# Kernel optimization log

Hardware: AMD Instinct MI355X
Metric: run time of the kernel (lower is better)

Reference implementation:

```python
import jax, jax.numpy as jnp
import numpy as np

EPS = 1e-5

def conv2d(x, w, b=None, pad=1):
    # x: [B,C,H,W], w: [O,I,kh,kw]
    y = jax.lax.conv_general_dilated(x, w, (1, 1), [(pad, pad), (pad, pad)],
                                     dimension_numbers=('NCHW', 'OIHW', 'NCHW'))
    if b is not None:
        y = y + b[None, :, None, None]
    return y

def bn(x, g, b, m, v):
    # inference-mode batchnorm
    inv = g / jnp.sqrt(v + EPS)
    return x * inv[None, :, None, None] + (b - m * inv)[None, :, None, None]

def coord_conv(x, w, b):
    B, C, H, W = x.shape
    yy = jnp.broadcast_to(jnp.linspace(-1.0, 1.0, H)[:, None], (H, W))
    xx = jnp.broadcast_to(jnp.linspace(-1.0, 1.0, W)[None, :], (H, W))
    coords = jnp.broadcast_to(jnp.stack([xx, yy])[None], (B, 2, H, W)).astype(x.dtype)
    return conv2d(jnp.concatenate([x, coords], axis=1), w, b, pad=1)

def deform_conv(x, offset, w):
    # deformable conv v1, 3x3, pad=1, stride=1, no bias
    B, C, H, W = x.shape
    K = 9
    # offset channels interleaved (y, x) per kernel tap
    off = offset.reshape(B, K, 2, H, W)
    off_y, off_x = off[:, :, 0], off[:, :, 1]          # [B,9,H,W]
    k = jnp.arange(K)
    ko_y = (k // 3 - 1).astype(x.dtype)[None, :, None, None]
    ko_x = (k % 3 - 1).astype(x.dtype)[None, :, None, None]
    base_y = jnp.arange(H, dtype=x.dtype)[None, None, :, None]
    base_x = jnp.arange(W, dtype=x.dtype)[None, None, None, :]
    py = base_y + ko_y + off_y                          # [B,9,H,W]
    px = base_x + ko_x + off_x
    xf = x.reshape(B, C, H * W)
    y0 = jnp.floor(py)
    x0 = jnp.floor(px)
    acc = jnp.zeros((B, C, K, H, W), x.dtype)
    for dy in (0.0, 1.0):
        for dx in (0.0, 1.0):
            yy = y0 + dy
            xx = x0 + dx
            wgt = (1.0 - jnp.abs(py - yy)) * (1.0 - jnp.abs(px - xx))
            valid = (yy >= 0) & (yy < H) & (xx >= 0) & (xx < W)
            wgt = jnp.where(valid, wgt, 0.0)            # zero padding OOB
            yi = jnp.clip(yy, 0, H - 1).astype(jnp.int32)
            xi = jnp.clip(xx, 0, W - 1).astype(jnp.int32)
            idx = (yi * W + xi).reshape(B, K * H * W)
            v = jnp.take_along_axis(xf, idx[:, None, :], axis=2).reshape(B, C, K, H, W)
            acc = acc + v * wgt[:, None]
    wk = w.reshape(w.shape[0], w.shape[1], K)           # [O,I,9]
    return jnp.einsum('bckhw,ock->bohw', acc, wk)

def setup_inputs() -> dict:
    key = jax.random.key(0)
    ks = jax.random.split(key, 16)
    d_model, hd = 256, 64
    B, H, W = 8, 96, 96
    f32 = jnp.float32
    def bn_params(k):
        k1, k2, k3 = jax.random.split(k, 3)
        return (1.0 + 0.1 * jax.random.normal(k1, (hd,), f32),
                0.1 * jax.random.normal(k2, (hd,), f32),
                0.1 * jax.random.normal(k3, (hd,), f32),
                0.5 + jax.random.uniform(jax.random.fold_in(k, 7), (hd,), f32))
    bn1 = bn_params(ks[1]); bn2 = bn_params(ks[2]); bn3 = bn_params(ks[3]); bn4 = bn_params(ks[4])
    inp = {
        'features': jax.random.normal(ks[0], (B, H, W, d_model), f32),
        'coord_w': 0.05 * jax.random.normal(ks[5], (hd, d_model + 2, 3, 3), f32),
        'coord_b': jnp.zeros((hd,), f32),
        'bn1_g': bn1[0], 'bn1_b': bn1[1], 'bn1_m': bn1[2], 'bn1_v': bn1[3],
        'off_w': 0.01 * jax.random.normal(ks[6], (18, hd, 3, 3), f32),
        'off_b': 0.01 * jax.random.normal(ks[7], (18,), f32),
        'dc_w': 0.05 * jax.random.normal(ks[8], (hd, hd, 3, 3), f32),
        'bn2_g': bn2[0], 'bn2_b': bn2[1], 'bn2_m': bn2[2], 'bn2_v': bn2[3],
        'r1_w': 0.05 * jax.random.normal(ks[9], (hd, hd, 3, 3), f32),
        'bn3_g': bn3[0], 'bn3_b': bn3[1], 'bn3_m': bn3[2], 'bn3_v': bn3[3],
        'r2_w': 0.05 * jax.random.normal(ks[10], (hd, hd, 3, 3), f32),
        'bn4_g': bn4[0], 'bn4_b': bn4[1], 'bn4_m': bn4[2], 'bn4_v': bn4[3],
        'out_w': 0.1 * jax.random.normal(ks[11], (1, hd, 1, 1), f32),
        'out_b': jnp.zeros((1,), f32),
    }
    return inp

def reference(features, coord_w, coord_b, bn1_g, bn1_b, bn1_m, bn1_v,
              off_w, off_b, dc_w, bn2_g, bn2_b, bn2_m, bn2_v,
              r1_w, bn3_g, bn3_b, bn3_m, bn3_v,
              r2_w, bn4_g, bn4_b, bn4_m, bn4_v, out_w, out_b):
    x = jnp.transpose(features, (0, 3, 1, 2))           # NHWC -> NCHW
    x = jax.nn.relu(bn(coord_conv(x, coord_w, coord_b), bn1_g, bn1_b, bn1_m, bn1_v))
    offset = conv2d(x, off_w, off_b, pad=1)
    x = deform_conv(x, offset, dc_w)
    x = jax.nn.relu(bn(x, bn2_g, bn2_b, bn2_m, bn2_v))
    x = jax.nn.relu(bn(conv2d(x, r1_w, None, pad=1), bn3_g, bn3_b, bn3_m, bn3_v))
    x = jax.nn.relu(bn(conv2d(x, r2_w, None, pad=1), bn4_g, bn4_b, bn4_m, bn4_v))
    return jax.nn.sigmoid(conv2d(x, out_w, out_b, pad=0))
```

## Files before the change

kernel.cpp:

```cpp
#include <hip/hip_runtime.h>


typedef unsigned short u16;
typedef unsigned int u32;
typedef __attribute__((ext_vector_type(8)))  short bf16x8;
typedef __attribute__((ext_vector_type(16))) float f32x16;

#define EPSBN 1e-5f

__device__ __forceinline__ u16 f2bf(float f) {
  u32 u = __builtin_bit_cast(u32, f);
  u32 r = u + 0x7FFFu + ((u >> 16) & 1u);
  return (u16)(r >> 16);
}
__device__ __forceinline__ u32 pk2(float a, float b) {
  return (u32)f2bf(a) | ((u32)f2bf(b) << 16);
}
__device__ __forceinline__ float lo2f(u32 w) { return __builtin_bit_cast(float, w << 16); }
__device__ __forceinline__ float hi2f(u32 w) { return __builtin_bit_cast(float, w & 0xFFFF0000u); }

__device__ __forceinline__ void gload_lds16(const void* g, void* l) {
  __builtin_amdgcn_global_load_lds(
      (const __attribute__((address_space(1))) unsigned int*)g,
      (__attribute__((address_space(3))) unsigned int*)l, 16, 0, 0);
}

#define N_WCF 147456
#define N_WCC 9216
#define N_WOF 18432
#define N_W64 36864
#define N_ALLW (N_WCF + N_WCC + N_WOF + 3*N_W64)

#define FBK_BLOCKS 9216
#define WT_BLOCKS  1116

__global__ __launch_bounds__(256) void prep_kernel(
    const float* __restrict__ feat,
    const float* __restrict__ coord_w, const float* __restrict__ off_w,
    const float* __restrict__ dc_w, const float* __restrict__ r1_w,
    const float* __restrict__ r2_w,
    u16* __restrict__ fb,
    u16* __restrict__ wcf, u16* __restrict__ wcc, u16* __restrict__ wof,
    u16* __restrict__ wdf, u16* __restrict__ wr1, u16* __restrict__ wr2,
    u32* __restrict__ zb)
{
  const int t = threadIdx.x;
  if (blockIdx.x < FBK_BLOCKS) {
    const int e = (blockIdx.x * 256 + t) * 8;
    const float4 f0 = *(const float4*)(feat + e);
    const float4 f1 = *(const float4*)(feat + e + 4);
    uint4 o;
    o.x = pk2(f0.x, f0.y); o.y = pk2(f0.z, f0.w);
    o.z = pk2(f1.x, f1.y); o.w = pk2(f1.z, f1.w);
    *(uint4*)(fb + e) = o;
    return;
  }
  int i = (blockIdx.x - FBK_BLOCKS) * 256 + t;
  if (i < 64) zb[i] = 0u;
  if (i >= N_ALLW) return;
  int d = i;
  if (d < N_WCF) {
    int j = d & 7, lane = (d >> 3) & 63, frag = d >> 9;
    int nt = frag & 1, h = (frag >> 1) & 3, tap = (frag >> 3) % 9, cc = (frag >> 3) / 9;
    int ic = cc * 64 + h * 16 + ((lane >> 5) << 3) + j;
    int oc = nt * 32 + (lane & 31);
    wcf[d] = f2bf(coord_w[((size_t)oc * 258 + ic) * 9 + tap]);
    return;
  }
  d -= N_WCF;
  if (d < N_WCC) {
    int j = d & 7, lane = (d >> 3) & 63, frag = d >> 9;
    int nt = frag & 1, tap = frag >> 1;
    int ic = 256 + ((lane >> 5) << 3) + j;
    int oc = nt * 32 + (lane & 31);
    wcc[d] = (ic < 258) ? f2bf(coord_w[((size_t)oc * 258 + ic) * 9 + tap]) : (u16)0;
    return;
  }
  d -= N_WCC;
  if (d < N_WOF) {
    int j = d & 7, lane = (d >> 3) & 63, frag = d >> 9;
    int h = frag & 3, tap = frag >> 2;
    int ic = h * 16 + ((lane >> 5) << 3) + j;
    int oc = lane & 31;
    wof[d] = (oc < 18) ? f2bf(off_w[((size_t)oc * 64 + ic) * 9 + tap]) : (u16)0;
    return;
  }
  d -= N_WOF;
  int seg = d / N_W64;
  int e = d - seg * N_W64;
  int j = e & 7, lane = (e >> 3) & 63, frag = e >> 9;
  int nt = frag & 1, h = (frag >> 1) & 3, tap = frag >> 3;
  int ic = h * 16 + ((lane >> 5) << 3) + j;
  int oc = nt * 32 + (lane & 31);
  const float* src = (seg == 0) ? dc_w : (seg == 1) ? r1_w : r2_w;
  u16* dst = (seg == 0) ? wdf : (seg == 1) ? wr1 : wr2;
  dst[e] = f2bf(src[((size_t)oc * 64 + ic) * 9 + tap]);
}

__device__ __forceinline__ u32 stage_desc(int slot, int x0, int y0, int b,
                                          int px_stride) {
  const int px = slot / 9, part = slot - px * 9;
  if (part >= 8 || px >= 204) return 0xFFFFFFFFu;
  const int ly = px / 34, lx = px - ly * 34;
  const int gy = y0 + ly - 1, gx = x0 + lx - 1;
  if ((unsigned)gy >= 96u || (unsigned)gx >= 96u) return 0xFFFFFFFFu;
  return (u32)(((b * 96 + gy) * 96 + gx) * px_stride + part * 16);
}

__global__ __launch_bounds__(256, 4) void coord_conv_kernel(
    const u16* __restrict__ fb, const u16* __restrict__ wcf,
    const u16* __restrict__ wcc, const float* __restrict__ cb,
    const float* __restrict__ g, const float* __restrict__ bb,
    const float* __restrict__ m, const float* __restrict__ v,
    u16* __restrict__ x1b, const u32* __restrict__ zb)
{
  __shared__ __align__(16) u16 tile[16384];
  __shared__ __align__(16) u16 ct[204 * 16];
  const int t = threadIdx.x;
  const int wv = t >> 6, lane = t & 63;
  const int l31 = lane & 31, l5 = lane >> 5;
  const int rp = wv & 1, kh = wv >> 1;
  const int x0 = blockIdx.x * 32, y0 = blockIdx.y * 4, b = blockIdx.z;

  u32 desc[8];
  #pragma unroll
  for (int k = 0; k < 8; ++k)
    desc[k] = stage_desc((wv + 4 * k) * 64 + lane, x0, y0, b, 512);

  if (t < 204) {
    const int ly = t / 34, lx = t - ly * 34;
    const int gy = y0 + ly - 1, gx = x0 + lx - 1;
    uint4 o0 = {0u, 0u, 0u, 0u}, o1 = {0u, 0u, 0u, 0u};
    if ((unsigned)gy < 96u && (unsigned)gx < 96u) {
      const float xx = -1.f + (2.f / 95.f) * (float)gx;
      const float yy = -1.f + (2.f / 95.f) * (float)gy;
      o0.x = pk2(xx, yy);
    }
    *(uint4*)(ct + t * 16) = o0;
    *(uint4*)(ct + t * 16 + 8) = o1;
  }

  f32x16 acc[2][2] = {};

  for (int cc = 0; cc < 4; ++cc) {
    #pragma unroll
    for (int k = 0; k < 8; ++k) {
      const char* src = (desc[k] == 0xFFFFFFFFu)
          ? (const char*)zb : (const char*)fb + desc[k] + cc * 128;
      gload_lds16(src, (char*)tile + (wv + 4 * k) * 1024);
    }
    __syncthreads();
    #pragma unroll
    for (int tap = 0; tap < 9; ++tap) {
      const int dy = tap / 3, dx = tap - dy * 3;
      #pragma unroll
      for (int hh = 0; hh < 2; ++hh) {
        const int h = kh * 2 + hh;
        const bf16x8 a0 = *(const bf16x8*)(tile +
            ((rp * 2 + 0 + dy) * 34 + l31 + dx) * 72 + h * 16 + l5 * 8);
        const bf16x8 a1 = *(const bf16x8*)(tile +
            ((rp * 2 + 1 + dy) * 34 + l31 + dx) * 72 + h * 16 + l5 * 8);
        #pragma unroll
        for (int nt = 0; nt < 2; ++nt) {
          const bf16x8 bfr = *(const bf16x8*)(wcf +
              ((size_t)((((cc * 9 + tap) * 4 + h) * 2) + nt)) * 512 + lane * 8);
          acc[0][nt] = __builtin_amdgcn_mfma_f32_32x32x16_bf16(a0, bfr,
                                                               acc[0][nt], 0, 0, 0);
          acc[1][nt] = __builtin_amdgcn_mfma_f32_32x32x16_bf16(a1, bfr,
                                                               acc[1][nt], 0, 0, 0);
        }
      }
    }
    __syncthreads();
  }

  if (kh == 0) {
    #pragma unroll
    for (int tap = 0; tap < 9; ++tap) {
      const int dy = tap / 3, dx = tap - dy * 3;
      const bf16x8 a0 = *(const bf16x8*)(ct +
          ((rp * 2 + 0 + dy) * 34 + l31 + dx) * 16 + l5 * 8);
      const bf16x8 a1 = *(const bf16x8*)(ct +
          ((rp * 2 + 1 + dy) * 34 + l31 + dx) * 16 + l5 * 8);
      #pragma unroll
      for (int nt = 0; nt < 2; ++nt) {
        const bf16x8 bfr = *(const bf16x8*)(wcc +
            ((size_t)(tap * 2 + nt)) * 512 + lane * 8);
        acc[0][nt] = __builtin_amdgcn_mfma_f32_32x32x16_bf16(a0, bfr,
                                                             acc[0][nt], 0, 0, 0);
        acc[1][nt] = __builtin_amdgcn_mfma_f32_32x32x16_bf16(a1, bfr,
                                                             acc[1][nt], 0, 0, 0);
      }
    }
  }

  float* redk = (float*)tile;
  __syncthreads();
  if (kh == 1) {
    #pragma unroll
    for (int ai = 0; ai < 2; ++ai)
      #pragma unroll
      for (int nt = 0; nt < 2; ++nt)
        #pragma unroll
        for (int r = 0; r < 16; ++r)
          redk[(((rp * 2 + ai) * 2 + nt) * 16 + r) * 64 + lane] = acc[ai][nt][r];
  }
  __syncthreads();
  if (kh == 0) {
    #pragma unroll
    for (int ai = 0; ai < 2; ++ai)
      #pragma unroll
      for (int nt = 0; nt < 2; ++nt) {
        #pragma unroll
        for (int r = 0; r < 16; ++r)
          acc[ai][nt][r] += redk[(((rp * 2 + ai) * 2 + nt) * 16 + r) * 64 + lane];
        const int oc = nt * 32 + l31;
        const float inv = g[oc] * rsqrtf(v[oc] + EPSBN);
        const float sh = bb[oc] - m[oc] * inv + cb[oc] * inv;
        const int y = y0 + rp * 2 + ai;
        #pragma unroll
        for (int r = 0; r < 16; ++r) {
          const int xr = (r & 3) + 8 * (r >> 2) + 4 * l5;
          const float val = fmaxf(fmaf(acc[ai][nt][r], inv, sh), 0.f);
          x1b[((size_t)((b * 96 + y) * 96 + x0 + xr)) * 64 + oc] = f2bf(val);
        }
      }
  }
}

template<int NN, int EPI>
__global__ __launch_bounds__(256, 4) void conv64_kernel(
    const u16* __restrict__ xin, const u16* __restrict__ wf,
    const float* __restrict__ bias,
    const float* __restrict__ g, const float* __restrict__ bb,
    const float* __restrict__ m, const float* __restrict__ v,
    const float* __restrict__ ow, const float* __restrict__ ob,
    void* __restrict__ outp, const u32* __restrict__ zb)
{
  __shared__ __align__(16) u16 tile[16384];
  __shared__ float red2[128];
  const int t = threadIdx.x;
  const int wv = t >> 6, lane = t & 63;
  const int l31 = lane & 31, l5 = lane >> 5;
  const int rp = wv & 1, kh = wv >> 1;
  const int x0 = blockIdx.x * 32, y0 = blockIdx.y * 4, b = blockIdx.z;

  #pragma unroll
  for (int k = 0; k < 8; ++k) {
    const u32 d = stage_desc((wv + 4 * k) * 64 + lane, x0, y0, b, 128);
    const char* src = (d == 0xFFFFFFFFu) ? (const char*)zb
                                         : (const char*)xin + d;
    gload_lds16(src, (char*)tile + (wv + 4 * k) * 1024);
  }
  __syncthreads();

  f32x16 acc[2][NN] = {};
  #pragma unroll
  for (int tap = 0; tap < 9; ++tap) {
    const int dy = tap / 3, dx = tap - dy * 3;
    #pragma unroll
    for (int hh = 0; hh < 2; ++hh) {
      const int h = kh * 2 + hh;
      const bf16x8 a0 = *(const bf16x8*)(tile +
          ((rp * 2 + 0 + dy) * 34 + l31 + dx) * 72 + h * 16 + l5 * 8);
      const bf16x8 a1 = *(const bf16x8*)(tile +
          ((rp * 2 + 1 + dy) * 34 + l31 + dx) * 72 + h * 16 + l5 * 8);
      #pragma unroll
      for (int nt = 0; nt < NN; ++nt) {
        const size_t f = (NN == 2) ? (size_t)((tap * 4 + h) * 2 + nt)
                                   : (size_t)(tap * 4 + h);
        const bf16x8 bfr = *(const bf16x8*)(wf + f * 512 + lane * 8);
        acc[0][nt] = __builtin_amdgcn_mfma_f32_32x32x16_bf16(a0, bfr,
                                                             acc[0][nt], 0, 0, 0);
        acc[1][nt] = __builtin_amdgcn_mfma_f32_32x32x16_bf16(a1, bfr,
                                                             acc[1][nt], 0, 0, 0);
      }
    }
  }

  float* redk = (float*)tile;
  __syncthreads();
  if (kh == 1) {
    #pragma unroll
    for (int ai = 0; ai < 2; ++ai)
      #pragma unroll
      for (int nt = 0; nt < NN; ++nt)
        #pragma unroll
        for (int r = 0; r < 16; ++r)
          redk[(((rp * 2 + ai) * NN + nt) * 16 + r) * 64 + lane] = acc[ai][nt][r];
  }
  __syncthreads();

  if constexpr (EPI == 0) {
    if (kh == 0) {
      u16* xo = (u16*)outp;
      #pragma unroll
      for (int ai = 0; ai < 2; ++ai)
        #pragma unroll
        for (int nt = 0; nt < NN; ++nt) {
          #pragma unroll
          for (int r = 0; r < 16; ++r)
            acc[ai][nt][r] += redk[(((rp * 2 + ai) * NN + nt) * 16 + r) * 64 + lane];
          const int oc = nt * 32 + l31;
          const float inv = g[oc] * rsqrtf(v[oc] + EPSBN);
          const float sh = bb[oc] - m[oc] * inv;
          const int y = y0 + rp * 2 + ai;
          #pragma unroll
          for (int r = 0; r < 16; ++r) {
            const int xr = (r & 3) + 8 * (r >> 2) + 4 * l5;
            const float val = fmaxf(fmaf(acc[ai][nt][r], inv, sh), 0.f);
            xo[((size_t)((b * 96 + y) * 96 + x0 + xr)) * 64 + oc] = f2bf(val);
          }
        }
    }
  } else if constexpr (EPI == 1) {
    if (kh == 0) {
      float* fo = (float*)outp;
      #pragma unroll
      for (int ai = 0; ai < 2; ++ai) {
        #pragma unroll
        for (int r = 0; r < 16; ++r)
          acc[ai][0][r] += redk[(((rp * 2 + ai) * NN + 0) * 16 + r) * 64 + lane];
        if (l31 < 18) {
          const float bs = bias[l31];
          const int y = y0 + rp * 2 + ai;
          #pragma unroll
          for (int r = 0; r < 16; ++r) {
            const int xr = (r & 3) + 8 * (r >> 2) + 4 * l5;
            fo[((size_t)((b * 96 + y) * 96 + x0 + xr)) * 18 + l31] =
                acc[ai][0][r] + bs;
          }
        }
      }
    }
  } else {
    if (kh == 0) {
      #pragma unroll
      for (int ai = 0; ai < 2; ++ai) {
        float pr[16];
        #pragma unroll
        for (int r = 0; r < 16; ++r) pr[r] = 0.f;
        #pragma unroll
        for (int nt = 0; nt < NN; ++nt) {
          const int oc = nt * 32 + l31;
          const float inv = g[oc] * rsqrtf(v[oc] + EPSBN);
          const float sh = bb[oc] - m[oc] * inv;
          const float wo = ow[oc];
          #pragma unroll
          for (int r = 0; r < 16; ++r) {
            const float a = acc[ai][nt][r] +
                redk[(((rp * 2 + ai) * NN + nt) * 16 + r) * 64 + lane];
            const float val = fmaxf(fmaf(a, inv, sh), 0.f);
            pr[r] = fmaf(val, wo, pr[r]);
          }
        }
        #pragma unroll
        for (int mask = 1; mask <= 16; mask <<= 1)
          #pragma unroll
          for (int r = 0; r < 16; ++r)
            pr[r] += __shfl_xor(pr[r], mask);
        if (l31 == 0) {
          #pragma unroll
          for (int r = 0; r < 16; ++r) {
            const int xr = (r & 3) + 8 * (r >> 2) + 4 * l5;
            red2[(rp * 2 + ai) * 32 + xr] = pr[r];
          }
        }
      }
    }
    __syncthreads();
    if (t < 128) {
      float* fo = (float*)outp;
      const int yy = y0 + (t >> 5), xx = x0 + (t & 31);
      const float val = red2[t] + ob[0];
      fo[(size_t)(b * 96 + yy) * 96 + xx] = 1.f / (1.f + expf(-val));
    }
  }
}

__global__ __launch_bounds__(512, 4) void deform_kernel(
    const u16* __restrict__ x1b, const float* __restrict__ off,
    const u16* __restrict__ wdf,
    const float* __restrict__ g, const float* __restrict__ bb,
    const float* __restrict__ m, const float* __restrict__ v,
    u16* __restrict__ x2b)
{
  __shared__ __align__(16) u16 s[2 * 128 * 72];
  __shared__ float offs[128 * 18];
  const int t = threadIdx.x;
  const int wv = t >> 6, lane = t & 63;
  const int l31 = lane & 31, l5 = lane >> 5;
  const int mt = wv & 3, ntw = wv >> 2;
  const int x0 = blockIdx.x * 16, y0 = blockIdx.y * 8, b = blockIdx.z;

  {
    float po[5];
    #pragma unroll
    for (int r = 0; r < 5; ++r) {
      const int i = t + r * 512;
      po[r] = 0.f;
      if (i < 2304) {
        const int p = i / 18, c = i - p * 18;
        const int gy = y0 + (p >> 4), gx = x0 + (p & 15);
        po[r] = off[((size_t)((b * 96 + gy) * 96 + gx)) * 18 + c];
      }
    }
    #pragma unroll
    for (int r = 0; r < 5; ++r) {
      const int i = t + r * 512;
      if (i < 2304) offs[i] = po[r];
    }
  }
  __syncthreads();

  const int sp = t >> 2, part = t & 3;
  const int sy = y0 + (sp >> 4), sx = x0 + (sp & 15);

  uint4 gbuf[8];
  float w4[4];

  auto prefetch = [&](int k) {
    const float oy = offs[sp * 18 + 2 * k];
    const float ox = offs[sp * 18 + 2 * k + 1];
    const float py = (float)(sy + k / 3 - 1) + oy;
    const float px = (float)(sx + k % 3 - 1) + ox;
    const float yf = floorf(py), xf = floorf(px);
    const float fy = py - yf, fx = px - xf;
    const int yi = (int)yf, xi = (int)xf;
    #pragma unroll
    for (int cor = 0; cor < 4; ++cor) {
      const int cy = yi + (cor >> 1), cx = xi + (cor & 1);
      const uint4 z = {0u, 0u, 0u, 0u};
      gbuf[2 * cor] = z; gbuf[2 * cor + 1] = z;
      const float wy = (cor & 2) ? fy : 1.f - fy;
      const float wx = (cor & 1) ? fx : 1.f - fx;
      w4[cor] = 0.f;
      if ((unsigned)cy < 96u && (unsigned)cx < 96u) {
        w4[cor] = wy * wx;
        const u16* p = x1b + ((size_t)((b * 96 + cy) * 96 + cx)) * 64
                       + part * 16;
        gbuf[2 * cor]     = *(const uint4*)p;
        gbuf[2 * cor + 1] = *(const uint4*)(p + 8);
      }
    }
  };
  auto combine = [&](u16* dst) {
    float val[16];
    #pragma unroll
    for (int j = 0; j < 16; ++j) val[j] = 0.f;
    #pragma unroll
    for (int cor = 0; cor < 4; ++cor) {
      const float wgt = w4[cor];
      const u32 uu[8] = {gbuf[2 * cor].x, gbuf[2 * cor].y,
                         gbuf[2 * cor].z, gbuf[2 * cor].w,
                         gbuf[2 * cor + 1].x, gbuf[2 * cor + 1].y,
                         gbuf[2 * cor + 1].z, gbuf[2 * cor + 1].w};
      #pragma unroll
      for (int u = 0; u < 8; ++u) {
        val[2 * u]     = fmaf(wgt, lo2f(uu[u]), val[2 * u]);
        val[2 * u + 1] = fmaf(wgt, hi2f(uu[u]), val[2 * u + 1]);
      }
    }
    u32 pk[8];
    #pragma unroll
    for (int u = 0; u < 8; ++u) pk[u] = pk2(val[2 * u], val[2 * u + 1]);
    uint4 w0 = {pk[0], pk[1], pk[2], pk[3]};
    uint4 w1 = {pk[4], pk[5], pk[6], pk[7]};
    *(uint4*)(dst + sp * 72 + part * 16) = w0;
    *(uint4*)(dst + sp * 72 + part * 16 + 8) = w1;
  };

  f32x16 acc = {};

  prefetch(0);
  combine(s);
  __syncthreads();

  for (int k = 0; k < 9; ++k) {
    u16* cur = s + (k & 1) * 9216;
    if (k < 8) prefetch(k + 1);
    #pragma unroll
    for (int h = 0; h < 4; ++h) {
      const bf16x8 afr = *(const bf16x8*)(cur + (mt * 32 + l31) * 72
                                          + h * 16 + l5 * 8);
      const bf16x8 bfr = *(const bf16x8*)(wdf +
          ((size_t)((k * 4 + h) * 2 + ntw)) * 512 + lane * 8);
      acc = __builtin_amdgcn_mfma_f32_32x32x16_bf16(afr, bfr, acc, 0, 0, 0);
    }
    if (k < 8) combine(s + ((k + 1) & 1) * 9216);
    __syncthreads();
  }

  const int oc = ntw * 32 + l31;
  const float inv = g[oc] * rsqrtf(v[oc] + EPSBN);
  const float sh = bb[oc] - m[oc] * inv;
  #pragma unroll
  for (int r = 0; r < 16; ++r) {
    const int pxi = mt * 32 + (r & 3) + 8 * (r >> 2) + 4 * l5;
    const int y = y0 + (pxi >> 4), x = x0 + (pxi & 15);
    const float val = fmaxf(fmaf(acc[r], inv, sh), 0.f);
    x2b[((size_t)((b * 96 + y) * 96 + x)) * 64 + oc] = f2bf(val);
  }
}

extern "C" void kernel_launch(void* const* d_in, const int* in_sizes, int n_in,
                              void* d_out, int out_size, void* d_ws,
                              size_t ws_size, hipStream_t stream)
{
  (void)in_sizes; (void)n_in; (void)out_size; (void)ws_size;
  const float* features = (const float*)d_in[0];
  const float* coord_w  = (const float*)d_in[1];
  const float* coord_b  = (const float*)d_in[2];
  const float* bn1g = (const float*)d_in[3];
  const float* bn1b = (const float*)d_in[4];
  const float* bn1m = (const float*)d_in[5];
  const float* bn1v = (const float*)d_in[6];
  const float* off_w = (const float*)d_in[7];
  const float* off_b = (const float*)d_in[8];
  const float* dc_w  = (const float*)d_in[9];
  const float* bn2g = (const float*)d_in[10];
  const float* bn2b = (const float*)d_in[11];
  const float* bn2m = (const float*)d_in[12];
  const float* bn2v = (const float*)d_in[13];
  const float* r1_w = (const float*)d_in[14];
  const float* bn3g = (const float*)d_in[15];
  const float* bn3b = (const float*)d_in[16];
  const float* bn3m = (const float*)d_in[17];
  const float* bn3v = (const float*)d_in[18];
  const float* r2_w = (const float*)d_in[19];
  const float* bn4g = (const float*)d_in[20];
  const float* bn4b = (const float*)d_in[21];
  const float* bn4m = (const float*)d_in[22];
  const float* bn4v = (const float*)d_in[23];
  const float* out_w = (const float*)d_in[24];
  const float* out_b = (const float*)d_in[25];

  char* W = (char*)d_ws;
  float* offb = (float*)W;
  u16*   x1b  = (u16*)(W + 5308416);
  u16*   x2b  = (u16*)(W + 14745600);
  u16*   x3b  = (u16*)(W + 24182784);
  u16*   wcf  = (u16*)(W + 33619968);
  u16*   wcc  = wcf + N_WCF;
  u16*   wof  = wcc + N_WCC;
  u16*   wdf  = wof + N_WOF;
  u16*   wr1  = wdf + N_W64;
  u16*   wr2  = wr1 + N_W64;
  u16*   fb   = (u16*)(W + 34191360);
  u32*   zb   = (u32*)(W + 71940096);

  prep_kernel<<<FBK_BLOCKS + WT_BLOCKS, 256, 0, stream>>>(
      features, coord_w, off_w, dc_w, r1_w, r2_w,
      fb, wcf, wcc, wof, wdf, wr1, wr2, zb);

  dim3 grid(3, 24, 8);
  dim3 gridD(6, 12, 8);

  coord_conv_kernel<<<grid, 256, 0, stream>>>(
      fb, wcf, wcc, coord_b, bn1g, bn1b, bn1m, bn1v, x1b, zb);
  conv64_kernel<1, 1><<<grid, 256, 0, stream>>>(
      x1b, wof, off_b, nullptr, nullptr, nullptr, nullptr, nullptr, nullptr,
      (void*)offb, zb);
  deform_kernel<<<gridD, 512, 0, stream>>>(
      x1b, offb, wdf, bn2g, bn2b, bn2m, bn2v, x2b);
  conv64_kernel<2, 0><<<grid, 256, 0, stream>>>(
      x2b, wr1, nullptr, bn3g, bn3b, bn3m, bn3v, nullptr, nullptr,
      (void*)x3b, zb);
  conv64_kernel<2, 2><<<grid, 256, 0, stream>>>(
      x3b, wr2, nullptr, bn4g, bn4b, bn4m, bn4v, out_w, out_b, d_out, zb);
}
```

Measured before the change: 282.1 us.

## Split conv waves by output-channel half, preload weights to registers, double-buffer coord tile

The coord conv and the 64-channel conv kernels now give each wave one 32-channel output half across all four rows, instead of two rows across both halves. Each wave preloads its B weight fragments into registers once, rather than reloading them from global memory inside the MFMA loop. The coord conv also double-buffers the LDS input tile so the next channel chunk's global-to-LDS copy overlaps compute. In exchange, register and LDS use grow, so launch bounds drop from 4 to 2 blocks per CU, which lowers occupancy.

```diff
diff --git a/kernel.cpp b/kernel.cpp
--- a/kernel.cpp
+++ b/kernel.cpp
@@ -107,19 +107,19 @@
   return (u32)(((b * 96 + gy) * 96 + gx) * px_stride + part * 16);
 }
 
-__global__ __launch_bounds__(256, 4) void coord_conv_kernel(
+__global__ __launch_bounds__(256, 2) void coord_conv_kernel(
     const u16* __restrict__ fb, const u16* __restrict__ wcf,
     const u16* __restrict__ wcc, const float* __restrict__ cb,
     const float* __restrict__ g, const float* __restrict__ bb,
     const float* __restrict__ m, const float* __restrict__ v,
     u16* __restrict__ x1b, const u32* __restrict__ zb)
 {
-  __shared__ __align__(16) u16 tile[16384];
+  __shared__ __align__(16) u16 tile[2][16384];
   __shared__ __align__(16) u16 ct[204 * 16];
   const int t = threadIdx.x;
   const int wv = t >> 6, lane = t & 63;
   const int l31 = lane & 31, l5 = lane >> 5;
-  const int rp = wv & 1, kh = wv >> 1;
+  const int ntw = wv & 1, kh = wv >> 1;
   const int x0 = blockIdx.x * 32, y0 = blockIdx.y * 4, b = blockIdx.z;
 
   u32 desc[8];
@@ -140,37 +140,50 @@
     *(uint4*)(ct + t * 16 + 8) = o1;
   }
 
-  f32x16 acc[2][2] = {};
-
-  for (int cc = 0; cc < 4; ++cc) {
+  bf16x8 wfr[18];
+  auto loadW = [&](int cc) {
+    #pragma unroll
+    for (int tap = 0; tap < 9; ++tap)
+      #pragma unroll
+      for (int hh = 0; hh < 2; ++hh)
+        wfr[tap * 2 + hh] = *(const bf16x8*)(wcf +
+            ((size_t)(((cc * 9 + tap) * 4 + kh * 2 + hh) * 2 + ntw)) * 512
+            + lane * 8);
+  };
+  auto issue = [&](int buf, int cc) {
     #pragma unroll
     for (int k = 0; k < 8; ++k) {
       const char* src = (desc[k] == 0xFFFFFFFFu)
           ? (const char*)zb : (const char*)fb + desc[k] + cc * 128;
-      gload_lds16(src, (char*)tile + (wv + 4 * k) * 1024);
-    }
-    __syncthreads();
+      gload_lds16(src, (char*)tile[buf] + (wv + 4 * k) * 1024);
+    }
+  };
+
+  f32x16 acc[4] = {};
+
+  issue(0, 0);
+  loadW(0);
+  __syncthreads();
+
+  for (int cc = 0; cc < 4; ++cc) {
+    if (cc < 3) issue((cc + 1) & 1, cc + 1);
+    const u16* tb = tile[cc & 1];
     #pragma unroll
     for (int tap = 0; tap < 9; ++tap) {
       const int dy = tap / 3, dx = tap - dy * 3;
       #pragma unroll
       for (int hh = 0; hh < 2; ++hh) {
-        const int h = kh * 2 + hh;
-        const bf16x8 a0 = *(const bf16x8*)(tile +
-            ((rp * 2 + 0 + dy) * 34 + l31 + dx) * 72 + h * 16 + l5 * 8);
-        const bf16x8 a1 = *(const bf16x8*)(tile +
-            ((rp * 2 + 1 + dy) * 34 + l31 + dx) * 72 + h * 16 + l5 * 8);
+        const bf16x8 bfr = wfr[tap * 2 + hh];
         #pragma unroll
-        for (int nt = 0; nt < 2; ++nt) {
-          const bf16x8 bfr = *(const bf16x8*)(wcf +
-              ((size_t)((((cc * 9 + tap) * 4 + h) * 2) + nt)) * 512 + lane * 8);
-          acc[0][nt] = __builtin_amdgcn_mfma_f32_32x32x16_bf16(a0, bfr,
-                                                               acc[0][nt], 0, 0, 0);
-          acc[1][nt] = __builtin_amdgcn_mfma_f32_32x32x16_bf16(a1, bfr,
-                                                               acc[1][nt], 0, 0, 0);
+        for (int ai = 0; ai < 4; ++ai) {
+          const bf16x8 a = *(const bf16x8*)(tb +
+              ((ai + dy) * 34 + l31 + dx) * 72 + (kh * 2 + hh) * 16 + l5 * 8);
+          acc[ai] = __builtin_amdgcn_mfma_f32_32x32x16_bf16(a, bfr, acc[ai],
+                                                            0, 0, 0);
         }
       }
     }
+    if (cc < 3) loadW(cc + 1);
     __syncthreads();
   }
 
@@ -178,58 +191,47 @@
     #pragma unroll
     for (int tap = 0; tap < 9; ++tap) {
       const int dy = tap / 3, dx = tap - dy * 3;
-      const bf16x8 a0 = *(const bf16x8*)(ct +
-          ((rp * 2 + 0 + dy) * 34 + l31 + dx) * 16 + l5 * 8);
-      const bf16x8 a1 = *(const bf16x8*)(ct +
-          ((rp * 2 + 1 + dy) * 34 + l31 + dx) * 16 + l5 * 8);
-      #pragma unroll
-      for (int nt = 0; nt < 2; ++nt) {
-        const bf16x8 bfr = *(const bf16x8*)(wcc +
-            ((size_t)(tap * 2 + nt)) * 512 + lane * 8);
-        acc[0][nt] = __builtin_amdgcn_mfma_f32_32x32x16_bf16(a0, bfr,
-                                                             acc[0][nt], 0, 0, 0);
-        acc[1][nt] = __builtin_amdgcn_mfma_f32_32x32x16_bf16(a1, bfr,
-                                                             acc[1][nt], 0, 0, 0);
-      }
-    }
-  }
-
-  float* redk = (float*)tile;
-  __syncthreads();
+      const bf16x8 bfr = *(const bf16x8*)(wcc +
+          ((size_t)(tap * 2 + ntw)) * 512 + lane * 8);
+      #pragma unroll
+      for (int ai = 0; ai < 4; ++ai) {
+        const bf16x8 a = *(const bf16x8*)(ct +
+            ((ai + dy) * 34 + l31 + dx) * 16 + l5 * 8);
+        acc[ai] = __builtin_amdgcn_mfma_f32_32x32x16_bf16(a, bfr, acc[ai],
+                                                          0, 0, 0);
+      }
+    }
+  }
+
+  float* redk = (float*)&tile[0][0];
   if (kh == 1) {
     #pragma unroll
-    for (int ai = 0; ai < 2; ++ai)
-      #pragma unroll
-      for (int nt = 0; nt < 2; ++nt)
-        #pragma unroll
-        for (int r = 0; r < 16; ++r)
-          redk[(((rp * 2 + ai) * 2 + nt) * 16 + r) * 64 + lane] = acc[ai][nt][r];
+    for (int ai = 0; ai < 4; ++ai)
+      #pragma unroll
+      for (int r = 0; r < 16; ++r)
+        redk[((ntw * 4 + ai) * 16 + r) * 64 + lane] = acc[ai][r];
   }
   __syncthreads();
   if (kh == 0) {
-    #pragma unroll
-    for (int ai = 0; ai < 2; ++ai)
-      #pragma unroll
-      for (int nt = 0; nt < 2; ++nt) {
-        #pragma unroll
-        for (int r = 0; r < 16; ++r)
-          acc[ai][nt][r] += redk[(((rp * 2 + ai) * 2 + nt) * 16 + r) * 64 + lane];
-        const int oc = nt * 32 + l31;
-        const float inv = g[oc] * rsqrtf(v[oc] + EPSBN);
-        const float sh = bb[oc] - m[oc] * inv + cb[oc] * inv;
-        const int y = y0 + rp * 2 + ai;
-        #pragma unroll
-        for (int r = 0; r < 16; ++r) {
-          const int xr = (r & 3) + 8 * (r >> 2) + 4 * l5;
-          const float val = fmaxf(fmaf(acc[ai][nt][r], inv, sh), 0.f);
-          x1b[((size_t)((b * 96 + y) * 96 + x0 + xr)) * 64 + oc] = f2bf(val);
-        }
-      }
+    const int oc = ntw * 32 + l31;
+    const float inv = g[oc] * rsqrtf(v[oc] + EPSBN);
+    const float sh = bb[oc] - m[oc] * inv + cb[oc] * inv;
+    #pragma unroll
+    for (int ai = 0; ai < 4; ++ai) {
+      const int y = y0 + ai;
+      #pragma unroll
+      for (int r = 0; r < 16; ++r) {
+        const float a = acc[ai][r] + redk[((ntw * 4 + ai) * 16 + r) * 64 + lane];
+        const int xr = (r & 3) + 8 * (r >> 2) + 4 * l5;
+        const float val = fmaxf(fmaf(a, inv, sh), 0.f);
+        x1b[((size_t)((b * 96 + y) * 96 + x0 + xr)) * 64 + oc] = f2bf(val);
+      }
+    }
   }
 }
 
 template<int NN, int EPI>
-__global__ __launch_bounds__(256, 4) void conv64_kernel(
+__global__ __launch_bounds__(256, 2) void conv64_kernel(
     const u16* __restrict__ xin, const u16* __restrict__ wf,
     const float* __restrict__ bias,
     const float* __restrict__ g, const float* __restrict__ bb,
@@ -238,11 +240,14 @@
     void* __restrict__ outp, const u32* __restrict__ zb)
 {
   __shared__ __align__(16) u16 tile[16384];
-  __shared__ float red2[128];
+  __shared__ float red2[2][128];
   const int t = threadIdx.x;
   const int wv = t >> 6, lane = t & 63;
   const int l31 = lane & 31, l5 = lane >> 5;
-  const int rp = wv & 1, kh = wv >> 1;
+  const int ntw = (NN == 2) ? (wv & 1) : 0;
+  const int rp  = (NN == 2) ? 0 : (wv & 1);
+  const int kh  = wv >> 1;
+  constexpr int NA = (NN == 2) ? 4 : 2;
   const int x0 = blockIdx.x * 32, y0 = blockIdx.y * 4, b = blockIdx.z;
 
   #pragma unroll
@@ -252,28 +257,32 @@
                                          : (const char*)xin + d;
     gload_lds16(src, (char*)tile + (wv + 4 * k) * 1024);
   }
-  __syncthreads();
-
-  f32x16 acc[2][NN] = {};
+  bf16x8 wfr[18];
+  #pragma unroll
+  for (int tap = 0; tap < 9; ++tap)
+    #pragma unroll
+    for (int hh = 0; hh < 2; ++hh) {
+      const int h = kh * 2 + hh;
+      const size_t f = (NN == 2) ? (size_t)((tap * 4 + h) * 2 + ntw)
+                                 : (size_t)(tap * 4 + h);
+      wfr[tap * 2 + hh] = *(const bf16x8*)(wf + f * 512 + lane * 8);
+    }
+  __syncthreads();
+
+  f32x16 acc[NA] = {};
   #pragma unroll
   for (int tap = 0; tap < 9; ++tap) {
     const int dy = tap / 3, dx = tap - dy * 3;
     #pragma unroll
     for (int hh = 0; hh < 2; ++hh) {
-      const int h = kh * 2 + hh;
-      const bf16x8 a0 = *(const bf16x8*)(tile +
-          ((rp * 2 + 0 + dy) * 34 + l31 + dx) * 72 + h * 16 + l5 * 8);
-      const bf16x8 a1 = *(const bf16x8*)(tile +
-          ((rp * 2 + 1 + dy) * 34 + l31 + dx) * 72 + h * 16 + l5 * 8);
-      #pragma unroll
-      for (int nt = 0; nt < NN; ++nt) {
-        const size_t f = (NN == 2) ? (size_t)((tap * 4 + h) * 2 + nt)
-                                   : (size_t)(tap * 4 + h);
-        const bf16x8 bfr = *(const bf16x8*)(wf + f * 512 + lane * 8);
-        acc[0][nt] = __builtin_amdgcn_mfma_f32_32x32x16_bf16(a0, bfr,
-                                                             acc[0][nt], 0, 0, 0);
-        acc[1][nt] = __builtin_amdgcn_mfma_f32_32x32x16_bf16(a1, bfr,
-                                                             acc[1][nt], 0, 0, 0);
+      const bf16x8 bfr = wfr[tap * 2 + hh];
+      #pragma unroll
+      for (int ai = 0; ai < NA; ++ai) {
+        const int rr = (NN == 2) ? ai : rp * 2 + ai;
+        const bf16x8 a = *(const bf16x8*)(tile +
+            ((rr + dy) * 34 + l31 + dx) * 72 + (kh * 2 + hh) * 16 + l5 * 8);
+        acc[ai] = __builtin_amdgcn_mfma_f32_32x32x16_bf16(a, bfr, acc[ai],
+                                                          0, 0, 0);
       }
     }
   }
@@ -282,77 +291,67 @@
   __syncthreads();
   if (kh == 1) {
     #pragma unroll
-    for (int ai = 0; ai < 2; ++ai)
-      #pragma unroll
-      for (int nt = 0; nt < NN; ++nt)
-        #pragma unroll
-        for (int r = 0; r < 16; ++r)
-          redk[(((rp * 2 + ai) * NN + nt) * 16 + r) * 64 + lane] = acc[ai][nt][r];
+    for (int ai = 0; ai < NA; ++ai) {
+      const int slot = (NN == 2) ? (ntw * 4 + ai) : (rp * 2 + ai);
+      #pragma unroll
+      for (int r = 0; r < 16; ++r)
+        redk[(slot * 16 + r) * 64 + lane] = acc[ai][r];
+    }
   }
   __syncthreads();
 
   if constexpr (EPI == 0) {
     if (kh == 0) {
       u16* xo = (u16*)outp;
-      #pragma unroll
-      for (int ai = 0; ai < 2; ++ai)
+      const int oc = ntw * 32 + l31;
+      const float inv = g[oc] * rsqrtf(v[oc] + EPSBN);
+      const float sh = bb[oc] - m[oc] * inv;
+      #pragma unroll
+      for (int ai = 0; ai < NA; ++ai) {
+        const int y = y0 + ai;
         #pragma unroll
-        for (int nt = 0; nt < NN; ++nt) {
-          #pragma unroll
-          for (int r = 0; r < 16; ++r)
-            acc[ai][nt][r] += redk[(((rp * 2 + ai) * NN + nt) * 16 + r) * 64 + lane];
-          const int oc = nt * 32 + l31;
-          const float inv = g[oc] * rsqrtf(v[oc] + EPSBN);
-          const float sh = bb[oc] - m[oc] * inv;
-          const int y = y0 + rp * 2 + ai;
+        for (int r = 0; r < 16; ++r) {
+          const float a = acc[ai][r] + redk[((ntw * 4 + ai) * 16 + r) * 64 + lane];
+          const int xr = (r & 3) + 8 * (r >> 2) + 4 * l5;
+          const float val = fmaxf(fmaf(a, inv, sh), 0.f);
+          xo[((size_t)((b * 96 + y) * 96 + x0 + xr)) * 64 + oc] = f2bf(val);
+        }
+      }
+    }
+  } else if constexpr (EPI == 1) {
+    if (kh == 0) {
+      float* fo = (float*)outp;
+      #pragma unroll
+      for (int ai = 0; ai < NA; ++ai) {
+        const int y = y0 + rp * 2 + ai;
+        float av[16];
+        #pragma unroll
+        for (int r = 0; r < 16; ++r)
+          av[r] = acc[ai][r] + redk[((rp * 2 + ai) * 16 + r) * 64 + lane];
+        if (l31 < 18) {
+          const float bs = bias[l31];
           #pragma unroll
           for (int r = 0; r < 16; ++r) {
             const int xr = (r & 3) + 8 * (r >> 2) + 4 * l5;
-            const float val = fmaxf(fmaf(acc[ai][nt][r], inv, sh), 0.f);
-            xo[((size_t)((b * 96 + y) * 96 + x0 + xr)) * 64 + oc] = f2bf(val);
+            fo[((size_t)((b * 96 + y) * 96 + x0 + xr)) * 18 + l31] = av[r] + bs;
           }
         }
-    }
-  } else if constexpr (EPI == 1) {
-    if (kh == 0) {
-      float* fo = (float*)outp;
-      #pragma unroll
-      for (int ai = 0; ai < 2; ++ai) {
-        #pragma unroll
-        for (int r = 0; r < 16; ++r)
-          acc[ai][0][r] += redk[(((rp * 2 + ai) * NN + 0) * 16 + r) * 64 + lane];
-        if (l31 < 18) {
-          const float bs = bias[l31];
-          const int y = y0 + rp * 2 + ai;
-          #pragma unroll
-          for (int r = 0; r < 16; ++r) {
-            const int xr = (r & 3) + 8 * (r >> 2) + 4 * l5;
-            fo[((size_t)((b * 96 + y) * 96 + x0 + xr)) * 18 + l31] =
-                acc[ai][0][r] + bs;
-          }
-        }
       }
     }
   } else {
     if (kh == 0) {
-      #pragma unroll
-      for (int ai = 0; ai < 2; ++ai) {
+      const int oc = ntw * 32 + l31;
+      const float inv = g[oc] * rsqrtf(v[oc] + EPSBN);
+      const float sh = bb[oc] - m[oc] * inv;
+      const float wo = ow[oc];
+      #pragma unroll
+      for (int ai = 0; ai < NA; ++ai) {
         float pr[16];
         #pragma unroll
-        for (int r = 0; r < 16; ++r) pr[r] = 0.f;
-        #pragma unroll
-        for (int nt = 0; nt < NN; ++nt) {
-          const int oc = nt * 32 + l31;
-          const float inv = g[oc] * rsqrtf(v[oc] + EPSBN);
-          const float sh = bb[oc] - m[oc] * inv;
-          const float wo = ow[oc];
-          #pragma unroll
-          for (int r = 0; r < 16; ++r) {
-            const float a = acc[ai][nt][r] +
-                redk[(((rp * 2 + ai) * NN + nt) * 16 + r) * 64 + lane];
-            const float val = fmaxf(fmaf(a, inv, sh), 0.f);
-            pr[r] = fmaf(val, wo, pr[r]);
-          }
+        for (int r = 0; r < 16; ++r) {
+          const float a = acc[ai][r] + redk[((ntw * 4 + ai) * 16 + r) * 64 + lane];
+          const float val = fmaxf(fmaf(a, inv, sh), 0.f);
+          pr[r] = val * wo;
         }
         #pragma unroll
         for (int mask = 1; mask <= 16; mask <<= 1)
@@ -363,7 +362,7 @@
           #pragma unroll
           for (int r = 0; r < 16; ++r) {
             const int xr = (r & 3) + 8 * (r >> 2) + 4 * l5;
-            red2[(rp * 2 + ai) * 32 + xr] = pr[r];
+            red2[ntw][ai * 32 + xr] = pr[r];
           }
         }
       }
@@ -372,7 +371,7 @@
     if (t < 128) {
       float* fo = (float*)outp;
       const int yy = y0 + (t >> 5), xx = x0 + (t & 31);
-      const float val = red2[t] + ob[0];
+      const float val = red2[0][t] + red2[1][t] + ob[0];
       fo[(size_t)(b * 96 + yy) * 96 + xx] = 1.f / (1.f + expf(-val));
     }
   }
```

New measurement: 268.5 us. -4.8%, faster.
